# Kernel optimization log

Measured on AMD Instinct MI355X. Metric: run time of the kernel, lower is better.

## Reference

```python
import jax, jax.numpy as jnp
import numpy as np

TAU = 0.2
N_CLUSTERS = 8
FOURIER_K = 8
LATENT_DIM = 64
B = 131072
N_MINUTES = 1440
TWO_PI = 2.0 * np.pi


def setup_inputs() -> dict:
    key = jax.random.key(0)
    ks = jax.random.split(key, 6)
    item_static_emb = jax.random.normal(ks[0], (B, LATENT_DIM), dtype=jnp.float32) * 0.1
    thetas = jax.random.uniform(ks[1], (B,), dtype=jnp.float32) * TWO_PI  # absolute time phase in [0, 2pi)
    cluster_prototypes = jax.random.normal(ks[2], (N_CLUSTERS, LATENT_DIM), dtype=jnp.float32) * 0.1
    fourier_a0 = jax.random.normal(ks[3], (N_CLUSTERS, LATENT_DIM), dtype=jnp.float32) * 0.1
    fourier_a = jax.random.normal(ks[4], (N_CLUSTERS, FOURIER_K, LATENT_DIM), dtype=jnp.float32) * 0.1
    fourier_b = jax.random.normal(ks[5], (N_CLUSTERS, FOURIER_K, LATENT_DIM), dtype=jnp.float32) * 0.1
    return {
        "item_static_emb": item_static_emb,
        "thetas": thetas,
        "cluster_prototypes": cluster_prototypes,
        "fourier_a0": fourier_a0,
        "fourier_a": fourier_a,
        "fourier_b": fourier_b,
    }


def reference(item_static_emb, thetas, cluster_prototypes, fourier_a0, fourier_a, fourier_b):
    # Soft cluster routing: (B, n_clusters)
    scores = jnp.matmul(item_static_emb, cluster_prototypes.T) / TAU
    P = jax.nn.softmax(scores, axis=1)

    # Time-indexed minute bucket; torch builds tables from linspace(0, 2pi, 1440)
    # so the angle for bucket m is m * 2pi/1439.
    minute_indices = jnp.clip((thetas / TWO_PI * N_MINUTES).astype(jnp.int32), 0, N_MINUTES - 1)
    k_seq = jnp.arange(1, FOURIER_K + 1, dtype=jnp.float32)  # (K,)
    angles = minute_indices.astype(jnp.float32) * (TWO_PI / (N_MINUTES - 1))  # (B,)
    k_angles = angles[:, None] * k_seq[None, :]  # (B, K)
    cos_vals = jnp.cos(k_angles)  # (B, K)
    sin_vals = jnp.sin(k_angles)  # (B, K)

    # Fourier-series evaluation per cluster: (B, n_clusters, d)
    a_term = jnp.einsum('bk,nkd->bnd', cos_vals, fourier_a)
    b_term = jnp.einsum('bk,nkd->bnd', sin_vals, fourier_b)
    F_theta = fourier_a0[None, :, :] + a_term + b_term  # (B, n_clusters, d)

    # Softmax-weighted mixture combine: (B, d)
    item_dynamic_emb = jnp.einsum('bn,bnd->bd', P, F_theta)
    return item_dynamic_emb, P
```

## Files before the change

### kernel.cpp

```cpp
#include <hip/hip_runtime.h>
#include <math.h>

#define D 64
#define NC 8
#define FK 8
#define NMIN 1440
#define TWO_PI_F 6.28318530717958647692f

__global__ __launch_bounds__(256) void build_table_kernel(
    const float* __restrict__ a0,
    const float* __restrict__ fa,
    const float* __restrict__ fb,
    float* __restrict__ T)
{
    const int m = blockIdx.x;
    const int t = threadIdx.x;
    const int d  = t & (D - 1);
    const int n0 = t >> 6;
    const float angle = (float)m * (TWO_PI_F / (float)(NMIN - 1));

    float c[FK], s[FK];
    float s1, c1;
    sincosf(angle, &s1, &c1);
    c[0] = c1; s[0] = s1;
    {
        const float tw = 2.0f * c1;
        float cp = 1.0f, sp = 0.0f;
        float cc = c1, ss = s1;
#pragma unroll
        for (int k = 1; k < FK; ++k) {
            const float cn = fmaf(tw, cc, -cp);
            const float sn = fmaf(tw, ss, -sp);
            cp = cc; sp = ss; cc = cn; ss = sn;
            c[k] = cc; s[k] = ss;
        }
    }

#pragma unroll
    for (int j = 0; j < 2; ++j) {
        const int n = n0 + 4 * j;
        float v = a0[n * D + d];
#pragma unroll
        for (int k = 0; k < FK; ++k) {
            v = fmaf(c[k], fa[(n * FK + k) * D + d], v);
            v = fmaf(s[k], fb[(n * FK + k) * D + d], v);
        }
        T[(m * NC + n) * D + d] = v;
    }
}

__device__ __forceinline__ float grp8_allreduce_sum(float v) {
    int t;
    t = __builtin_amdgcn_update_dpp(0, __float_as_int(v), 0xB1, 0xF, 0xF, true);
    v += __int_as_float(t);
    t = __builtin_amdgcn_update_dpp(0, __float_as_int(v), 0x4E, 0xF, 0xF, true);
    v += __int_as_float(t);
    t = __builtin_amdgcn_update_dpp(0, __float_as_int(v), 0x141, 0xF, 0xF, true);
    v += __int_as_float(t);
    return v;
}

__global__ __launch_bounds__(256) void mix_kernel8(
    const float* __restrict__ emb,
    const float* __restrict__ thetas,
    const float* __restrict__ proto,
    const float* __restrict__ T,
    float* __restrict__ out_emb,
    float* __restrict__ out_P,
    int B)
{
    __shared__ float4 sproto[NC * (D / 4)];
    if (threadIdx.x < NC * (D / 4)) {
        sproto[threadIdx.x] = ((const float4*)proto)[threadIdx.x];
    }
    __syncthreads();

    const int t = blockIdx.x * 256 + threadIdx.x;
    const int b = t >> 3;
    const int j = t & 7;
    if (b >= B) return;

    const float th = thetas[b];
    int m = (int)((th / TWO_PI_F) * (float)NMIN);
    m = m < 0 ? 0 : (m > NMIN - 1 ? NMIN - 1 : m);

    const float4* __restrict__ e4 = (const float4*)emb + (size_t)b * (D / 4);
    const float4 ev0 = e4[j];
    const float4 ev1 = e4[j + 8];

    float sc[NC];
#pragma unroll
    for (int n = 0; n < NC; ++n) {
        const float4 pa = sproto[n * (D / 4) + j];
        const float4 pb = sproto[n * (D / 4) + j + 8];
        float v = ev0.x * pa.x;
        v = fmaf(ev0.y, pa.y, v);
        v = fmaf(ev0.z, pa.z, v);
        v = fmaf(ev0.w, pa.w, v);
        v = fmaf(ev1.x, pb.x, v);
        v = fmaf(ev1.y, pb.y, v);
        v = fmaf(ev1.z, pb.z, v);
        v = fmaf(ev1.w, pb.w, v);
        sc[n] = v;
    }

#pragma unroll
    for (int n = 0; n < NC; ++n) {
        sc[n] = grp8_allreduce_sum(sc[n]);
    }

    float mx = -1e30f;
#pragma unroll
    for (int n = 0; n < NC; ++n) { sc[n] *= 5.0f; mx = fmaxf(mx, sc[n]); }
    float sum = 0.0f;
#pragma unroll
    for (int n = 0; n < NC; ++n) { sc[n] = __expf(sc[n] - mx); sum += sc[n]; }
    const float inv = 1.0f / sum;
#pragma unroll
    for (int n = 0; n < NC; ++n) sc[n] *= inv;

    const float4* __restrict__ t4 = (const float4*)(T + (size_t)m * NC * D);
    float4 acc0 = make_float4(0.f, 0.f, 0.f, 0.f);
    float4 acc1 = make_float4(0.f, 0.f, 0.f, 0.f);
#pragma unroll
    for (int n = 0; n < NC; ++n) {
        const float4 ta = t4[n * (D / 4) + j];
        const float4 tb = t4[n * (D / 4) + j + 8];
        const float pw = sc[n];
        acc0.x = fmaf(pw, ta.x, acc0.x);
        acc0.y = fmaf(pw, ta.y, acc0.y);
        acc0.z = fmaf(pw, ta.z, acc0.z);
        acc0.w = fmaf(pw, ta.w, acc0.w);
        acc1.x = fmaf(pw, tb.x, acc1.x);
        acc1.y = fmaf(pw, tb.y, acc1.y);
        acc1.z = fmaf(pw, tb.z, acc1.z);
        acc1.w = fmaf(pw, tb.w, acc1.w);
    }

    float4* __restrict__ o4 = (float4*)out_emb + (size_t)b * (D / 4);
    o4[j]     = acc0;
    o4[j + 8] = acc1;

    if (j == 0) {
        ((float4*)out_P)[(size_t)b * 2 + 0] = make_float4(sc[0], sc[1], sc[2], sc[3]);
    } else if (j == 4) {
        ((float4*)out_P)[(size_t)b * 2 + 1] = make_float4(sc[4], sc[5], sc[6], sc[7]);
    }
}

__global__ __launch_bounds__(256) void fused_fallback(
    const float* __restrict__ emb,
    const float* __restrict__ thetas,
    const float* __restrict__ proto,
    const float* __restrict__ a0,
    const float* __restrict__ fa,
    const float* __restrict__ fb,
    float* __restrict__ out_emb,
    float* __restrict__ out_P,
    int B)
{
    __shared__ float sp[NC * D];
    __shared__ float sa0[NC * D];
    __shared__ float sfa[NC * FK * D];
    __shared__ float sfb[NC * FK * D];
    for (int i = threadIdx.x; i < NC * D; i += 256) { sp[i] = proto[i]; sa0[i] = a0[i]; }
    for (int i = threadIdx.x; i < NC * FK * D; i += 256) { sfa[i] = fa[i]; sfb[i] = fb[i]; }
    __syncthreads();

    const int b = blockIdx.x * 256 + threadIdx.x;
    if (b >= B) return;

    const float4* __restrict__ e4  = (const float4*)(emb + (size_t)b * D);
    const float4* sp4  = (const float4*)sp;
    const float4* sa04 = (const float4*)sa0;
    const float4* sfa4 = (const float4*)sfa;
    const float4* sfb4 = (const float4*)sfb;

    float sc[NC];
#pragma unroll
    for (int n = 0; n < NC; ++n) sc[n] = 0.0f;
#pragma unroll
    for (int i = 0; i < D / 4; ++i) {
        const float4 ev = e4[i];
#pragma unroll
        for (int n = 0; n < NC; ++n) {
            const float4 pv = sp4[n * (D / 4) + i];
            sc[n] = fmaf(ev.x, pv.x, sc[n]);
            sc[n] = fmaf(ev.y, pv.y, sc[n]);
            sc[n] = fmaf(ev.z, pv.z, sc[n]);
            sc[n] = fmaf(ev.w, pv.w, sc[n]);
        }
    }
    float mx = -1e30f;
#pragma unroll
    for (int n = 0; n < NC; ++n) { sc[n] *= 5.0f; mx = fmaxf(mx, sc[n]); }
    float sum = 0.0f;
#pragma unroll
    for (int n = 0; n < NC; ++n) { sc[n] = __expf(sc[n] - mx); sum += sc[n]; }
    const float inv = 1.0f / sum;
#pragma unroll
    for (int n = 0; n < NC; ++n) sc[n] *= inv;

    const float th = thetas[b];
    int m = (int)((th / TWO_PI_F) * (float)NMIN);
    m = m < 0 ? 0 : (m > NMIN - 1 ? NMIN - 1 : m);
    const float angle = (float)m * (TWO_PI_F / (float)(NMIN - 1));
    float c[FK], s[FK];
#pragma unroll
    for (int k = 0; k < FK; ++k) sincosf(angle * (float)(k + 1), &s[k], &c[k]);

    float4 acc[D / 4];
#pragma unroll
    for (int i = 0; i < D / 4; ++i) acc[i] = make_float4(0.f, 0.f, 0.f, 0.f);
#pragma unroll
    for (int n = 0; n < NC; ++n) {
        const float pw = sc[n];
#pragma unroll
        for (int i = 0; i < D / 4; ++i) {
            float4 v = sa04[n * (D / 4) + i];
#pragma unroll
            for (int k = 0; k < FK; ++k) {
                const float4 av = sfa4[(n * FK + k) * (D / 4) + i];
                const float4 bv = sfb4[(n * FK + k) * (D / 4) + i];
                v.x = fmaf(c[k], av.x, v.x); v.x = fmaf(s[k], bv.x, v.x);
                v.y = fmaf(c[k], av.y, v.y); v.y = fmaf(s[k], bv.y, v.y);
                v.z = fmaf(c[k], av.z, v.z); v.z = fmaf(s[k], bv.z, v.z);
                v.w = fmaf(c[k], av.w, v.w); v.w = fmaf(s[k], bv.w, v.w);
            }
            acc[i].x = fmaf(pw, v.x, acc[i].x);
            acc[i].y = fmaf(pw, v.y, acc[i].y);
            acc[i].z = fmaf(pw, v.z, acc[i].z);
            acc[i].w = fmaf(pw, v.w, acc[i].w);
        }
    }
    float4* o4 = (float4*)(out_emb + (size_t)b * D);
#pragma unroll
    for (int i = 0; i < D / 4; ++i) o4[i] = acc[i];
    float4* op = (float4*)(out_P + (size_t)b * NC);
    op[0] = make_float4(sc[0], sc[1], sc[2], sc[3]);
    op[1] = make_float4(sc[4], sc[5], sc[6], sc[7]);
}

extern "C" void kernel_launch(void* const* d_in, const int* in_sizes, int n_in,
                              void* d_out, int out_size, void* d_ws, size_t ws_size,
                              hipStream_t stream)
{
    const float* emb    = (const float*)d_in[0];
    const float* thetas = (const float*)d_in[1];
    const float* proto  = (const float*)d_in[2];
    const float* a0     = (const float*)d_in[3];
    const float* fa     = (const float*)d_in[4];
    const float* fb     = (const float*)d_in[5];

    const int B = in_sizes[0] / D;
    float* out_emb = (float*)d_out;
    float* out_P   = (float*)d_out + (size_t)B * D;

    const size_t table_bytes = (size_t)NMIN * NC * D * sizeof(float);

    if (ws_size >= table_bytes) {
        float* T = (float*)d_ws;
        build_table_kernel<<<NMIN, 256, 0, stream>>>(a0, fa, fb, T);
        const long long total_threads = (long long)B * 8;
        const int blocks = (int)((total_threads + 255) / 256);
        mix_kernel8<<<blocks, 256, 0, stream>>>(emb, thetas, proto, T, out_emb, out_P, B);
    } else {
        const int blocks = (B + 255) / 256;
        fused_fallback<<<blocks, 256, 0, stream>>>(emb, thetas, proto, a0, fa, fb,
                                                   out_emb, out_P, B);
    }
}
```

Measured before the change: 30.68 us.

## Bucket items by minute index so each block reuses one table slice

```diff
diff --git a/kernel.cpp b/kernel.cpp
--- a/kernel.cpp
+++ b/kernel.cpp
@@ -5,7 +5,10 @@
 #define NC 8
 #define FK 8
 #define NMIN 1440
+#define SLOTCAP 256
 #define TWO_PI_F 6.28318530717958647692f
+
+#define TSZ ((size_t)NMIN * NC * D)
 
 __global__ __launch_bounds__(256) void build_table_kernel(
     const float* __restrict__ a0,
@@ -45,8 +48,23 @@
             v = fmaf(c[k], fa[(n * FK + k) * D + d], v);
             v = fmaf(s[k], fb[(n * FK + k) * D + d], v);
         }
-        T[(m * NC + n) * D + d] = v;
-    }
+        T[(size_t)(m * NC + n) * D + d] = v;
+    }
+}
+
+__global__ __launch_bounds__(256) void bucket_kernel(
+    const float* __restrict__ thetas,
+    int* __restrict__ cnt,
+    int* __restrict__ slots,
+    int B)
+{
+    const int b = blockIdx.x * 256 + threadIdx.x;
+    if (b >= B) return;
+    const float th = thetas[b];
+    int m = (int)((th / TWO_PI_F) * (float)NMIN);
+    m = m < 0 ? 0 : (m > NMIN - 1 ? NMIN - 1 : m);
+    const int pos = atomicAdd(&cnt[m], 1);
+    if (pos < SLOTCAP) slots[m * SLOTCAP + pos] = b;
 }
 
 __device__ __forceinline__ float grp8_allreduce_sum(float v) {
@@ -60,14 +78,14 @@
     return v;
 }
 
-__global__ __launch_bounds__(256) void mix_kernel8(
+__global__ __launch_bounds__(256) void mix_bucket_kernel(
     const float* __restrict__ emb,
-    const float* __restrict__ thetas,
     const float* __restrict__ proto,
     const float* __restrict__ T,
+    const int* __restrict__ cnt,
+    const int* __restrict__ slots,
     float* __restrict__ out_emb,
-    float* __restrict__ out_P,
-    int B)
+    float* __restrict__ out_P)
 {
     __shared__ float4 sproto[NC * (D / 4)];
     if (threadIdx.x < NC * (D / 4)) {
@@ -75,76 +93,79 @@
     }
     __syncthreads();
 
-    const int t = blockIdx.x * 256 + threadIdx.x;
-    const int b = t >> 3;
-    const int j = t & 7;
-    if (b >= B) return;
-
-    const float th = thetas[b];
-    int m = (int)((th / TWO_PI_F) * (float)NMIN);
-    m = m < 0 ? 0 : (m > NMIN - 1 ? NMIN - 1 : m);
-
-    const float4* __restrict__ e4 = (const float4*)emb + (size_t)b * (D / 4);
-    const float4 ev0 = e4[j];
-    const float4 ev1 = e4[j + 8];
-
-    float sc[NC];
-#pragma unroll
-    for (int n = 0; n < NC; ++n) {
-        const float4 pa = sproto[n * (D / 4) + j];
-        const float4 pb = sproto[n * (D / 4) + j + 8];
-        float v = ev0.x * pa.x;
-        v = fmaf(ev0.y, pa.y, v);
-        v = fmaf(ev0.z, pa.z, v);
-        v = fmaf(ev0.w, pa.w, v);
-        v = fmaf(ev1.x, pb.x, v);
-        v = fmaf(ev1.y, pb.y, v);
-        v = fmaf(ev1.z, pb.z, v);
-        v = fmaf(ev1.w, pb.w, v);
-        sc[n] = v;
-    }
-
-#pragma unroll
-    for (int n = 0; n < NC; ++n) {
-        sc[n] = grp8_allreduce_sum(sc[n]);
-    }
-
-    float mx = -1e30f;
-#pragma unroll
-    for (int n = 0; n < NC; ++n) { sc[n] *= 5.0f; mx = fmaxf(mx, sc[n]); }
-    float sum = 0.0f;
-#pragma unroll
-    for (int n = 0; n < NC; ++n) { sc[n] = __expf(sc[n] - mx); sum += sc[n]; }
-    const float inv = 1.0f / sum;
-#pragma unroll
-    for (int n = 0; n < NC; ++n) sc[n] *= inv;
-
+    const int m = blockIdx.x;
+    int count = cnt[m];
+    if (count > SLOTCAP) count = SLOTCAP;
+
+    const int g = threadIdx.x >> 3;
+    const int j = threadIdx.x & 7;
     const float4* __restrict__ t4 = (const float4*)(T + (size_t)m * NC * D);
-    float4 acc0 = make_float4(0.f, 0.f, 0.f, 0.f);
-    float4 acc1 = make_float4(0.f, 0.f, 0.f, 0.f);
-#pragma unroll
-    for (int n = 0; n < NC; ++n) {
-        const float4 ta = t4[n * (D / 4) + j];
-        const float4 tb = t4[n * (D / 4) + j + 8];
-        const float pw = sc[n];
-        acc0.x = fmaf(pw, ta.x, acc0.x);
-        acc0.y = fmaf(pw, ta.y, acc0.y);
-        acc0.z = fmaf(pw, ta.z, acc0.z);
-        acc0.w = fmaf(pw, ta.w, acc0.w);
-        acc1.x = fmaf(pw, tb.x, acc1.x);
-        acc1.y = fmaf(pw, tb.y, acc1.y);
-        acc1.z = fmaf(pw, tb.z, acc1.z);
-        acc1.w = fmaf(pw, tb.w, acc1.w);
-    }
-
-    float4* __restrict__ o4 = (float4*)out_emb + (size_t)b * (D / 4);
-    o4[j]     = acc0;
-    o4[j + 8] = acc1;
-
-    if (j == 0) {
-        ((float4*)out_P)[(size_t)b * 2 + 0] = make_float4(sc[0], sc[1], sc[2], sc[3]);
-    } else if (j == 4) {
-        ((float4*)out_P)[(size_t)b * 2 + 1] = make_float4(sc[4], sc[5], sc[6], sc[7]);
+    const int* __restrict__ bslots = slots + m * SLOTCAP;
+
+    for (int it = g; it < count; it += 32) {
+        const int b = bslots[it];
+
+        const float4* __restrict__ e4 = (const float4*)emb + (size_t)b * (D / 4);
+        const float4 ev0 = e4[j];
+        const float4 ev1 = e4[j + 8];
+
+        float sc[NC];
+#pragma unroll
+        for (int n = 0; n < NC; ++n) {
+            const float4 pa = sproto[n * (D / 4) + j];
+            const float4 pb = sproto[n * (D / 4) + j + 8];
+            float v = ev0.x * pa.x;
+            v = fmaf(ev0.y, pa.y, v);
+            v = fmaf(ev0.z, pa.z, v);
+            v = fmaf(ev0.w, pa.w, v);
+            v = fmaf(ev1.x, pb.x, v);
+            v = fmaf(ev1.y, pb.y, v);
+            v = fmaf(ev1.z, pb.z, v);
+            v = fmaf(ev1.w, pb.w, v);
+            sc[n] = v;
+        }
+
+#pragma unroll
+        for (int n = 0; n < NC; ++n) {
+            sc[n] = grp8_allreduce_sum(sc[n]);
+        }
+
+        float mx = -1e30f;
+#pragma unroll
+        for (int n = 0; n < NC; ++n) { sc[n] *= 5.0f; mx = fmaxf(mx, sc[n]); }
+        float sum = 0.0f;
+#pragma unroll
+        for (int n = 0; n < NC; ++n) { sc[n] = __expf(sc[n] - mx); sum += sc[n]; }
+        const float inv = 1.0f / sum;
+#pragma unroll
+        for (int n = 0; n < NC; ++n) sc[n] *= inv;
+
+        float4 acc0 = make_float4(0.f, 0.f, 0.f, 0.f);
+        float4 acc1 = make_float4(0.f, 0.f, 0.f, 0.f);
+#pragma unroll
+        for (int n = 0; n < NC; ++n) {
+            const float4 ta = t4[n * (D / 4) + j];
+            const float4 tb = t4[n * (D / 4) + j + 8];
+            const float pw = sc[n];
+            acc0.x = fmaf(pw, ta.x, acc0.x);
+            acc0.y = fmaf(pw, ta.y, acc0.y);
+            acc0.z = fmaf(pw, ta.z, acc0.z);
+            acc0.w = fmaf(pw, ta.w, acc0.w);
+            acc1.x = fmaf(pw, tb.x, acc1.x);
+            acc1.y = fmaf(pw, tb.y, acc1.y);
+            acc1.z = fmaf(pw, tb.z, acc1.z);
+            acc1.w = fmaf(pw, tb.w, acc1.w);
+        }
+
+        float4* __restrict__ o4 = (float4*)out_emb + (size_t)b * (D / 4);
+        o4[j]     = acc0;
+        o4[j + 8] = acc1;
+
+        if (j == 0) {
+            ((float4*)out_P)[(size_t)b * 2 + 0] = make_float4(sc[0], sc[1], sc[2], sc[3]);
+        } else if (j == 4) {
+            ((float4*)out_P)[(size_t)b * 2 + 1] = make_float4(sc[4], sc[5], sc[6], sc[7]);
+        }
     }
 }
 
@@ -256,14 +277,20 @@
     float* out_emb = (float*)d_out;
     float* out_P   = (float*)d_out + (size_t)B * D;
 
-    const size_t table_bytes = (size_t)NMIN * NC * D * sizeof(float);
-
-    if (ws_size >= table_bytes) {
-        float* T = (float*)d_ws;
+    const size_t need_bytes = TSZ * sizeof(float)
+                            + (size_t)NMIN * sizeof(int)
+                            + (size_t)NMIN * SLOTCAP * sizeof(int);
+
+    if (ws_size >= need_bytes) {
+        float* T    = (float*)d_ws;
+        int* cnt    = (int*)(T + TSZ);
+        int* slots  = cnt + NMIN;
+
+        hipMemsetAsync(cnt, 0, (size_t)NMIN * sizeof(int), stream);
         build_table_kernel<<<NMIN, 256, 0, stream>>>(a0, fa, fb, T);
-        const long long total_threads = (long long)B * 8;
-        const int blocks = (int)((total_threads + 255) / 256);
-        mix_kernel8<<<blocks, 256, 0, stream>>>(emb, thetas, proto, T, out_emb, out_P, B);
+        bucket_kernel<<<(B + 255) / 256, 256, 0, stream>>>(thetas, cnt, slots, B);
+        mix_bucket_kernel<<<NMIN, 256, 0, stream>>>(emb, proto, T, cnt, slots,
+                                                    out_emb, out_P);
     } else {
         const int blocks = (B + 255) / 256;
         fused_fallback<<<blocks, 256, 0, stream>>>(emb, thetas, proto, a0, fa, fb,
```

Result: slower. 53.92 us (+75.7%).
